# Kernel optimization log

Measured on AMD Instinct MI355X. Metric: run time of the kernel, lower is better.

The kernel has to match this reference:

```python
import jax, jax.numpy as jnp
import numpy as np
from jax.scipy.special import digamma

K_NEIGHBOURS = 5  # matches init_kwargs nNeighbours


def setup_inputs() -> dict:
    key = jax.random.key(0)
    k1, k2 = jax.random.split(key)
    x = jax.random.normal(k1, (2, 2, 64, 64), dtype=jnp.float32)
    y = jax.random.normal(k2, (2, 2, 64, 64), dtype=jnp.float32)
    return {"x": x, "y": y}


def _knn_mi(x, y, k):
    # KSG k-NN mutual information estimator, channel-wise.
    B, C, H, W = x.shape
    BC, HW = B * C, H * W
    xv = x.reshape(BC, HW)
    yv = y.reshape(BC, HW)
    # Pairwise L1 (scalar -> abs diff) distance matrices: (BC, HW, HW)
    dx = jnp.abs(xv[:, :, None] - xv[:, None, :])
    dy = jnp.abs(yv[:, :, None] - yv[:, None, :])
    # Joint-space Chebyshev distance (max over the two marginals)
    z = jnp.maximum(dx, dy)
    # eps = (k+1)-th smallest joint distance per point (includes self-distance 0),
    # matching torch .topk(k+1, largest=False).values[..., -1:]
    neg_smallest = jax.lax.top_k(-z, k + 1)[0]       # (BC, HW, k+1), descending in -z
    eps = -neg_smallest[:, :, -1:]                    # (BC, HW, 1)
    # Marginal neighbor counts with strict < eps (self included, as in torch code)
    nx = jnp.sum(dx < eps, axis=-1).astype(jnp.float32)  # (BC, HW)
    ny = jnp.sum(dy < eps, axis=-1).astype(jnp.float32)
    const = digamma(jnp.float32(k)) + digamma(jnp.float32(HW))
    mi = const - jnp.mean(digamma(nx) + digamma(ny), axis=-1)  # (BC,)
    return jnp.maximum(mi.reshape(B, C), 0.0)


def reference(x, y):
    return _knn_mi(x, y, K_NEIGHBOURS)
```

## Files before the change

kernel.cpp:

```cpp
#include <hip/hip_runtime.h>
#include <math.h>

#define HW 4096
#define NCH 4
#define TPB 256
#define ROWS_PER_BLOCK 16
#define BLOCKS_PER_CH 256
#define NBLOCKS (NCH * BLOCKS_PER_CH)
#define KNN 5
#define WINB 544

#define NBINS 512
#define BLO   (-6.0f)
#define BDELTA 0.0234375f
#define BINV  (512.0f / 12.0f)
#define SLOP  1e-5f
#define INFT  3.4e38f

#define WS_BXY   16384
#define WS_BY    32768
#define WS_PREF  49152
#define WS_PART  57344

__device__ __forceinline__ int binOf(float v) {
    int b = (int)floorf((v - BLO) * BINV);
    return min(max(b, 0), NBINS - 1);
}

__device__ __forceinline__ float digammaf_dev(float x) {
    float r = 0.f;
    while (x < 6.f) { r -= 1.f / x; x += 1.f; }
    float f = 1.f / x, f2 = f * f;
    return logf(x) - 0.5f * f
         - f2 * (1.f / 12.f - f2 * (1.f / 120.f - f2 * (1.f / 252.f))) + r;
}

__device__ __forceinline__ void insert6(float (&s)[6], float d) {
    float n0 = fminf(s[0], d);
    float n1 = __builtin_amdgcn_fmed3f(s[0], s[1], d);
    float n2 = __builtin_amdgcn_fmed3f(s[1], s[2], d);
    float n3 = __builtin_amdgcn_fmed3f(s[2], s[3], d);
    float n4 = __builtin_amdgcn_fmed3f(s[3], s[4], d);
    float n5 = __builtin_amdgcn_fmed3f(s[4], s[5], d);
    s[0] = n0; s[1] = n1; s[2] = n2; s[3] = n3; s[4] = n4; s[5] = n5;
}

__global__ __launch_bounds__(256) void knnmi_bucketize(const float* __restrict__ x,
                                                       const float* __restrict__ y,
                                                       float* __restrict__ ws) {
    __shared__ int h[NBINS];
    const int c    = blockIdx.x >> 1;
    const int side = blockIdx.x & 1;
    const int t    = threadIdx.x;
    const float* src  = (side == 0 ? x : y) + c * HW;
    const float* ysrc = y + c * HW;
    int* pref = (int*)ws + WS_PREF + (side ? NCH * (NBINS + 1) : 0) + c * (NBINS + 1);

    for (int i = t; i < NBINS; i += 256) h[i] = 0;
    __syncthreads();

    float vx[16], vy[16];
    int bn[16];
#pragma unroll
    for (int k = 0; k < 16; ++k) {
        int i = t + k * 256;
        float v = src[i];
        vx[k] = v;
        vy[k] = (side == 0) ? ysrc[i] : 0.f;
        bn[k] = binOf(v);
        atomicAdd(&h[bn[k]], 1);
    }
    __syncthreads();

    if (t < 64) {
        int sinc[8];
        {
            sinc[0] = h[t * 8 + 0];
#pragma unroll
            for (int j = 1; j < 8; ++j) sinc[j] = sinc[j - 1] + h[t * 8 + j];
        }
        int tot = sinc[7], inc = tot;
#pragma unroll
        for (int off = 1; off < 64; off <<= 1) {
            int u = __shfl_up(inc, off);
            if (t >= off) inc += u;
        }
        int ex = inc - tot;
#pragma unroll
        for (int j = 0; j < 8; ++j) {
            int st = ex + (j ? sinc[j - 1] : 0);
            h[t * 8 + j]    = st;
            pref[t * 8 + j] = st;
        }
        if (t == 63) pref[NBINS] = HW;
    }
    __syncthreads();

    if (side == 0) {
        float* bxx = ws + c * HW;
        float* bxy = ws + WS_BXY + c * HW;
#pragma unroll
        for (int k = 0; k < 16; ++k) {
            int pos = atomicAdd(&h[bn[k]], 1);
            bxx[pos] = vx[k];
            bxy[pos] = vy[k];
        }
    } else {
        float* by = ws + WS_BY + c * HW;
#pragma unroll
        for (int k = 0; k < 16; ++k) {
            int pos = atomicAdd(&h[bn[k]], 1);
            by[pos] = vx[k];
        }
    }
}

__global__ __launch_bounds__(TPB, 6) void knnmi_rows(float* __restrict__ ws) {
    __shared__ float2 swin[WINB];
    __shared__ int pfy[NBINS + 1];
    __shared__ float red[ROWS_PER_BLOCK];

    const int c  = blockIdx.x >> 8;
    const int rb = blockIdx.x & 255;
    const int R0 = rb * ROWS_PER_BLOCK;
    const float* bxx = ws + c * HW;
    const float* bxy = ws + WS_BXY + c * HW;
    const float* by  = ws + WS_BY  + c * HW;
    const int* prefy = (const int*)ws + WS_PREF + NCH * (NBINS + 1) + c * (NBINS + 1);

    int LO = R0 - 264;
    LO = max(LO, 0); LO = min(LO, HW - WINB); LO &= ~3;
    const int HI = LO + WINB;

    const float xLm1 = (LO > 0)  ? bxx[LO - 1] : 0.f;
    const float xHIv = (HI < HW) ? bxx[HI]     : 0.f;

    if (threadIdx.x < WINB / 4) {
        float4 xv = ((const float4*)(bxx + LO))[threadIdx.x];
        float4 yv = ((const float4*)(bxy + LO))[threadIdx.x];
        ((float4*)swin)[2 * threadIdx.x]     = make_float4(xv.x, yv.x, xv.y, yv.y);
        ((float4*)swin)[2 * threadIdx.x + 1] = make_float4(xv.z, yv.z, xv.w, yv.w);
    }
    for (int i = threadIdx.x; i <= NBINS; i += TPB) pfy[i] = prefy[i];
    __syncthreads();

    const int wv   = threadIdx.x >> 6;
    const int lane = threadIdx.x & 63;
    const int l    = lane & 15;
    const int g    = lane >> 4;
    const int q    = wv * 4 + g;
    const int p    = R0 + q;

    const float xi = swin[p - LO].x;
    const float yi = swin[p - LO].y;

    float s[6];
#pragma unroll
    for (int k = 0; k < 6; ++k) s[k] = INFT;

    const float4* f4 = (const float4*)swin;
#pragma unroll 4
    for (int it = 0; it < WINB / 32; ++it) {
        float4 pp = f4[it * 16 + l];
        insert6(s, fmaxf(fabsf(xi - pp.x), fabsf(yi - pp.y)));
        insert6(s, fmaxf(fabsf(xi - pp.z), fabsf(yi - pp.w)));
    }

#pragma unroll
    for (int m = 1; m < 16; m <<= 1) {
        float o[6];
#pragma unroll
        for (int k = 0; k < 6; ++k) o[k] = __shfl_xor(s[k], m);
#pragma unroll
        for (int k = 0; k < 6; ++k) insert6(s, o[k]);
    }
    float eps = s[5];

    float eL = INFT, eR = INFT;
    if (LO > 0) {
        int b = binOf(xLm1);
        eL = xi - (BLO + (float)(b + 1) * BDELTA + SLOP);
    }
    if (HI < HW) {
        int b = binOf(xHIv);
        eR = (BLO + (float)b * BDELTA - SLOP) - xi;
    }
    const bool ok = (eps <= eL) && (eps <= eR);

    int nx = 0, ny = 0;
    bool fell = false;
    unsigned long long bad = __ballot((l == 0) && !ok);
    while (bad) {
        int bit = (int)__ffsll(bad) - 1;
        bad &= bad - 1;
        const int tg = bit >> 4;
        const float xt = swin[(R0 + wv * 4 + tg) - LO].x;
        const float yt = swin[(R0 + wv * 4 + tg) - LO].y;
        float s3[6];
#pragma unroll
        for (int k = 0; k < 6; ++k) s3[k] = INFT;
        for (int it = 0; it < HW / 256; ++it) {
            float4 xv = ((const float4*)bxx)[it * 64 + lane];
            float4 yv = ((const float4*)bxy)[it * 64 + lane];
            insert6(s3, fmaxf(fabsf(xt - xv.x), fabsf(yt - yv.x)));
            insert6(s3, fmaxf(fabsf(xt - xv.y), fabsf(yt - yv.y)));
            insert6(s3, fmaxf(fabsf(xt - xv.z), fabsf(yt - yv.z)));
            insert6(s3, fmaxf(fabsf(xt - xv.w), fabsf(yt - yv.w)));
        }
#pragma unroll
        for (int m = 1; m < 64; m <<= 1) {
            float o[6];
#pragma unroll
            for (int k = 0; k < 6; ++k) o[k] = __shfl_xor(s3[k], m);
#pragma unroll
            for (int k = 0; k < 6; ++k) insert6(s3, o[k]);
        }
        const float e3 = s3[5];
        int cx = 0, cy = 0;
        for (int it = 0; it < HW / 256; ++it) {
            float4 xv = ((const float4*)bxx)[it * 64 + lane];
            float4 yv = ((const float4*)bxy)[it * 64 + lane];
            cx += (fabsf(xt - xv.x) < e3) + (fabsf(xt - xv.y) < e3)
                + (fabsf(xt - xv.z) < e3) + (fabsf(xt - xv.w) < e3);
            cy += (fabsf(yt - yv.x) < e3) + (fabsf(yt - yv.y) < e3)
                + (fabsf(yt - yv.z) < e3) + (fabsf(yt - yv.w) < e3);
        }
        int pk3 = (cx << 16) | cy;
#pragma unroll
        for (int m = 1; m < 64; m <<= 1) pk3 += __shfl_xor(pk3, m);
        if (g == tg) { eps = e3; nx = pk3 >> 16; ny = pk3 & 0xffff; fell = true; }
    }

    if (!fell) {
#pragma unroll 4
        for (int it = 0; it < WINB / 32; ++it) {
            float4 pp = f4[it * 16 + l];
            nx += (fabsf(xi - pp.x) < eps) + (fabsf(xi - pp.z) < eps);
        }
        int loB = binOf(yi - eps), hiB = binOf(yi + eps);
        int fLo = loB + 2, fHi = hiB - 2;
        if (fLo <= fHi) {
            if (l == 0) ny += pfy[fHi + 1] - pfy[fLo];
            int a0 = pfy[max(loB - 1, 0)], a1 = pfy[min(loB + 1, NBINS - 1) + 1];
            int b0 = pfy[max(hiB - 1, 0)], b1 = pfy[min(hiB + 1, NBINS - 1) + 1];
            for (int tt = a0 + l; tt < a1; tt += 16) ny += (fabsf(by[tt] - yi) < eps);
            for (int tt = b0 + l; tt < b1; tt += 16) ny += (fabsf(by[tt] - yi) < eps);
        } else {
            int a0 = pfy[max(loB - 1, 0)], a1 = pfy[min(hiB + 1, NBINS - 1) + 1];
            for (int tt = a0 + l; tt < a1; tt += 16) ny += (fabsf(by[tt] - yi) < eps);
        }
    }

    if (fell && l != 0) { nx = 0; ny = 0; }
    int pk = (nx << 16) | ny;
#pragma unroll
    for (int m = 1; m < 16; m <<= 1) pk += __shfl_xor(pk, m);

    if (l == 0)
        red[q] = digammaf_dev((float)(pk >> 16)) + digammaf_dev((float)(pk & 0xffff));
    __syncthreads();

    if (threadIdx.x == 0) {
        float v = 0.f;
#pragma unroll
        for (int k = 0; k < ROWS_PER_BLOCK; ++k) v += red[k];
        (ws + WS_PART)[blockIdx.x] = v;
    }
}

__global__ void knnmi_final(const float* __restrict__ ws, float* __restrict__ out) {
    const float* partials = ws + WS_PART;
    const int w    = threadIdx.x >> 6;
    const int lane = threadIdx.x & 63;
    float sum = 0.f;
#pragma unroll
    for (int i = lane; i < BLOCKS_PER_CH; i += 64)
        sum += partials[w * BLOCKS_PER_CH + i];
#pragma unroll
    for (int m = 32; m; m >>= 1) sum += __shfl_xor(sum, m);
    if (lane == 0) {
        float mi = digammaf_dev((float)KNN) + digammaf_dev((float)HW)
                 - sum / (float)HW;
        out[w] = fmaxf(mi, 0.f);
    }
}

extern "C" void kernel_launch(void* const* d_in, const int* in_sizes, int n_in,
                              void* d_out, int out_size, void* d_ws, size_t ws_size,
                              hipStream_t stream) {
    const float* x = (const float*)d_in[0];
    const float* y = (const float*)d_in[1];
    float* out = (float*)d_out;
    float* ws  = (float*)d_ws;

    knnmi_bucketize<<<2 * NCH, 256, 0, stream>>>(x, y, ws);
    knnmi_rows<<<NBLOCKS, TPB, 0, stream>>>(ws);
    knnmi_final<<<1, NCH * 64, 0, stream>>>(ws, out);
}
```

Baseline: 33.61 us.

## Use 32 lanes per row with dual top-6 lists and smaller window

Each query row is now handled by 32 lanes instead of 16, so a block covers 8 rows and twice as many blocks are launched. The candidate window shrinks from 544 to 512 points, and the scan keeps two independent top-6 lists that are merged at the end to shorten dependency chains. Occupancy hint raised to 8 blocks. The trade-offs are a longer shuffle-merge tree per row, more blocks that each reload the window and prefix array, and a narrower window that may send more rows down the slow full-scan fallback.

```diff
diff --git a/kernel.cpp b/kernel.cpp
--- a/kernel.cpp
+++ b/kernel.cpp
@@ -4,11 +4,12 @@
 #define HW 4096
 #define NCH 4
 #define TPB 256
-#define ROWS_PER_BLOCK 16
-#define BLOCKS_PER_CH 256
+#define G 32
+#define ROWS_PER_BLOCK 8
+#define BLOCKS_PER_CH (HW / ROWS_PER_BLOCK)
 #define NBLOCKS (NCH * BLOCKS_PER_CH)
 #define KNN 5
-#define WINB 544
+#define WINB 512
 
 #define NBINS 512
 #define BLO   (-6.0f)
@@ -115,20 +116,20 @@
     }
 }
 
-__global__ __launch_bounds__(TPB, 6) void knnmi_rows(float* __restrict__ ws) {
+__global__ __launch_bounds__(TPB, 8) void knnmi_rows(float* __restrict__ ws) {
     __shared__ float2 swin[WINB];
     __shared__ int pfy[NBINS + 1];
     __shared__ float red[ROWS_PER_BLOCK];
 
-    const int c  = blockIdx.x >> 8;
-    const int rb = blockIdx.x & 255;
+    const int c  = blockIdx.x >> 9;
+    const int rb = blockIdx.x & 511;
     const int R0 = rb * ROWS_PER_BLOCK;
     const float* bxx = ws + c * HW;
     const float* bxy = ws + WS_BXY + c * HW;
     const float* by  = ws + WS_BY  + c * HW;
     const int* prefy = (const int*)ws + WS_PREF + NCH * (NBINS + 1) + c * (NBINS + 1);
 
-    int LO = R0 - 264;
+    int LO = R0 - 252;
     LO = max(LO, 0); LO = min(LO, HW - WINB); LO &= ~3;
     const int HI = LO + WINB;
 
@@ -146,35 +147,37 @@
 
     const int wv   = threadIdx.x >> 6;
     const int lane = threadIdx.x & 63;
-    const int l    = lane & 15;
-    const int g    = lane >> 4;
-    const int q    = wv * 4 + g;
+    const int l    = lane & (G - 1);
+    const int g    = lane >> 5;
+    const int q    = wv * 2 + g;
     const int p    = R0 + q;
 
     const float xi = swin[p - LO].x;
     const float yi = swin[p - LO].y;
 
-    float s[6];
-#pragma unroll
-    for (int k = 0; k < 6; ++k) s[k] = INFT;
+    float sa[6], sb[6];
+#pragma unroll
+    for (int k = 0; k < 6; ++k) { sa[k] = INFT; sb[k] = INFT; }
 
     const float4* f4 = (const float4*)swin;
-#pragma unroll 4
-    for (int it = 0; it < WINB / 32; ++it) {
-        float4 pp = f4[it * 16 + l];
-        insert6(s, fmaxf(fabsf(xi - pp.x), fabsf(yi - pp.y)));
-        insert6(s, fmaxf(fabsf(xi - pp.z), fabsf(yi - pp.w)));
-    }
-
-#pragma unroll
-    for (int m = 1; m < 16; m <<= 1) {
+#pragma unroll
+    for (int it = 0; it < WINB / (2 * G); ++it) {
+        float4 pp = f4[it * G + l];
+        insert6(sa, fmaxf(fabsf(xi - pp.x), fabsf(yi - pp.y)));
+        insert6(sb, fmaxf(fabsf(xi - pp.z), fabsf(yi - pp.w)));
+    }
+#pragma unroll
+    for (int k = 0; k < 6; ++k) insert6(sa, sb[k]);
+
+#pragma unroll
+    for (int m = 1; m < G; m <<= 1) {
         float o[6];
 #pragma unroll
-        for (int k = 0; k < 6; ++k) o[k] = __shfl_xor(s[k], m);
-#pragma unroll
-        for (int k = 0; k < 6; ++k) insert6(s, o[k]);
-    }
-    float eps = s[5];
+        for (int k = 0; k < 6; ++k) o[k] = __shfl_xor(sa[k], m);
+#pragma unroll
+        for (int k = 0; k < 6; ++k) insert6(sa, o[k]);
+    }
+    float eps = sa[5];
 
     float eL = INFT, eR = INFT;
     if (LO > 0) {
@@ -193,9 +196,9 @@
     while (bad) {
         int bit = (int)__ffsll(bad) - 1;
         bad &= bad - 1;
-        const int tg = bit >> 4;
-        const float xt = swin[(R0 + wv * 4 + tg) - LO].x;
-        const float yt = swin[(R0 + wv * 4 + tg) - LO].y;
+        const int tg = bit >> 5;
+        const float xt = swin[(R0 + wv * 2 + tg) - LO].x;
+        const float yt = swin[(R0 + wv * 2 + tg) - LO].y;
         float s3[6];
 #pragma unroll
         for (int k = 0; k < 6; ++k) s3[k] = INFT;
@@ -232,9 +235,9 @@
     }
 
     if (!fell) {
-#pragma unroll 4
-        for (int it = 0; it < WINB / 32; ++it) {
-            float4 pp = f4[it * 16 + l];
+#pragma unroll
+        for (int it = 0; it < WINB / (2 * G); ++it) {
+            float4 pp = f4[it * G + l];
             nx += (fabsf(xi - pp.x) < eps) + (fabsf(xi - pp.z) < eps);
         }
         int loB = binOf(yi - eps), hiB = binOf(yi + eps);
@@ -243,18 +246,18 @@
             if (l == 0) ny += pfy[fHi + 1] - pfy[fLo];
             int a0 = pfy[max(loB - 1, 0)], a1 = pfy[min(loB + 1, NBINS - 1) + 1];
             int b0 = pfy[max(hiB - 1, 0)], b1 = pfy[min(hiB + 1, NBINS - 1) + 1];
-            for (int tt = a0 + l; tt < a1; tt += 16) ny += (fabsf(by[tt] - yi) < eps);
-            for (int tt = b0 + l; tt < b1; tt += 16) ny += (fabsf(by[tt] - yi) < eps);
+            for (int tt = a0 + l; tt < a1; tt += G) ny += (fabsf(by[tt] - yi) < eps);
+            for (int tt = b0 + l; tt < b1; tt += G) ny += (fabsf(by[tt] - yi) < eps);
         } else {
             int a0 = pfy[max(loB - 1, 0)], a1 = pfy[min(hiB + 1, NBINS - 1) + 1];
-            for (int tt = a0 + l; tt < a1; tt += 16) ny += (fabsf(by[tt] - yi) < eps);
+            for (int tt = a0 + l; tt < a1; tt += G) ny += (fabsf(by[tt] - yi) < eps);
         }
     }
 
     if (fell && l != 0) { nx = 0; ny = 0; }
     int pk = (nx << 16) | ny;
 #pragma unroll
-    for (int m = 1; m < 16; m <<= 1) pk += __shfl_xor(pk, m);
+    for (int m = 1; m < G; m <<= 1) pk += __shfl_xor(pk, m);
 
     if (l == 0)
         red[q] = digammaf_dev((float)(pk >> 16)) + digammaf_dev((float)(pk & 0xffff));
```

After: 34.20 us. No clear change (+1.8%).
